# Optimization experiments

Hardware: AMD Instinct MI355X
Metric: run time of the kernel (lower is better)

## Reference

```python
import jax, jax.numpy as jnp
import numpy as np
import math

LMAX = 3  # max output/input angular momentum degree


def _cg(j1, m1, j2, m2, j, m):
    """Clebsch-Gordan coefficient <j1 m1 j2 m2 | j m> (Condon-Shortley)."""
    if m1 + m2 != m or not (abs(j1 - j2) <= j <= j1 + j2):
        return 0.0
    f = math.factorial
    pref = math.sqrt(
        (2 * j + 1)
        * f(j + j1 - j2) * f(j - j1 + j2) * f(j1 + j2 - j) / f(j1 + j2 + j + 1)
        * f(j + m) * f(j - m) * f(j1 - m1) * f(j1 + m1) * f(j2 - m2) * f(j2 + m2)
    )
    kmin = max(0, j2 - j - m1, j1 - j + m2)
    kmax = min(j1 + j2 - j, j1 - m1, j2 + m2)
    s = 0.0
    for k in range(kmin, kmax + 1):
        s += (-1) ** k / (
            f(k) * f(j1 + j2 - j - k) * f(j1 - m1 - k) * f(j2 + m2 - k)
            * f(j - j2 + m1 + k) * f(j - j1 - m2 + k)
        )
    return pref * s


def _cg_mat(l1, l2, l):
    C = np.zeros((2 * l1 + 1, 2 * l2 + 1, 2 * l + 1), dtype=np.float32)
    for m1 in range(-l1, l1 + 1):
        for m2 in range(-l2, l2 + 1):
            m = m1 + m2
            if abs(m) <= l:
                C[m1 + l1, m2 + l2, m + l] = _cg(l1, m1, l2, m2, l, m)
    return C


_CG = {}
for _l1 in range(LMAX + 1):
    for _l2 in range(LMAX + 1):
        for _l in range(abs(_l1 - _l2), min(_l1 + _l2, LMAX) + 1):
            _CG[(_l1, _l2, _l)] = jnp.asarray(_cg_mat(_l1, _l2, _l))


def _cg_product(A, B):
    """Full CG tensor product of two SO3 vec-arrays.

    A[l], B[l]: (2=complex, N, 2l+1, tau). Output degree l collects, for every
    (l1, l2) pair with |l1-l2| <= l <= l1+l2, the channel outer product
    contracted against the CG matrix (cormorant CGProduct semantics).
    """
    parts = [[] for _ in range(LMAX + 1)]
    for l1 in range(LMAX + 1):
        for l2 in range(LMAX + 1):
            Ar, Ai = A[l1][0], A[l1][1]  # (N, 2l1+1, tau1)
            Br, Bi = B[l2][0], B[l2][1]  # (N, 2l2+1, tau2)
            for l in range(abs(l1 - l2), min(l1 + l2, LMAX) + 1):
                C = _CG[(l1, l2, l)]  # (2l1+1, 2l2+1, 2l+1)
                Tr = (jnp.einsum('xyz,nxc,nyd->nzcd', C, Ar, Br)
                      - jnp.einsum('xyz,nxc,nyd->nzcd', C, Ai, Bi))
                Ti = (jnp.einsum('xyz,nxc,nyd->nzcd', C, Ar, Bi)
                      + jnp.einsum('xyz,nxc,nyd->nzcd', C, Ai, Br))
                n = Tr.shape[0]
                T = jnp.stack([Tr, Ti], axis=0).reshape(2, n, 2 * l + 1, -1)
                parts[l].append(T)
    return tuple(jnp.concatenate(p, axis=-1) for p in parts)


def setup_inputs() -> dict:
    key = jax.random.key(0)
    keys = jax.random.split(key, 8)
    N, TAU = 1024, 16
    d = {}
    for l in range(LMAX + 1):
        d[f'A{l}'] = jax.random.normal(keys[l], (2, N, 2 * l + 1, TAU), dtype=jnp.float32)
        d[f'B{l}'] = jax.random.normal(keys[4 + l], (2, N, 2 * l + 1, TAU), dtype=jnp.float32)
    return d


def reference(A0, A1, A2, A3, B0, B1, B2, B3):
    return _cg_product([A0, A1, A2, A3], [B0, B1, B2, B3])
```

## Files before the change

kernel.cpp:

```cpp
#include <hip/hip_runtime.h>


typedef float f32x4 __attribute__((ext_vector_type(4)));

constexpr double dfactc(int n) {
    double r = 1.0;
    for (int i = 2; i <= n; ++i) r *= (double)i;
    return r;
}

constexpr double csqrt(double x) {
    if (x <= 0.0) return 0.0;
    double g = x >= 1.0 ? x : 1.0;
    for (int i = 0; i < 50; ++i) g = 0.5 * (g + x / g);
    return g;
}

constexpr double cg_coef_c(int j1, int m1, int j2, int m2, int j, int m) {
    if (m1 + m2 != m) return 0.0;
    double pref = csqrt((double)(2 * j + 1)
        * dfactc(j + j1 - j2) * dfactc(j - j1 + j2) * dfactc(j1 + j2 - j)
        / dfactc(j1 + j2 + j + 1)
        * dfactc(j + m) * dfactc(j - m) * dfactc(j1 - m1) * dfactc(j1 + m1)
        * dfactc(j2 - m2) * dfactc(j2 + m2));
    int kmin = 0;
    if (j2 - j - m1 > kmin) kmin = j2 - j - m1;
    if (j1 - j + m2 > kmin) kmin = j1 - j + m2;
    int kmax = j1 + j2 - j;
    if (j1 - m1 < kmax) kmax = j1 - m1;
    if (j2 + m2 < kmax) kmax = j2 + m2;
    double s = 0.0;
    for (int k = kmin; k <= kmax; ++k) {
        double d = dfactc(k) * dfactc(j1 + j2 - j - k) * dfactc(j1 - m1 - k)
                 * dfactc(j2 + m2 - k) * dfactc(j - j2 + m1 + k)
                 * dfactc(j - j1 - m2 + k);
        s += (k & 1) ? (-1.0 / d) : (1.0 / d);
    }
    return pref * s;
}

template <int l1, int l2, int L>
struct CGMat {
    float v[(2 * l1 + 1) * (2 * l2 + 1) * (2 * L + 1)];
};

template <int l1, int l2, int L>
constexpr CGMat<l1, l2, L> make_cgmat() {
    CGMat<l1, l2, L> t{};
    constexpr int yd = 2 * l2 + 1, zd = 2 * L + 1;
    for (int x = 0; x < 2 * l1 + 1; ++x)
        for (int y = 0; y < yd; ++y)
            for (int z = 0; z < zd; ++z)
                t.v[(x * yd + y) * zd + z] =
                    (float)cg_coef_c(l1, x - l1, l2, y - l2, L, z - L);
    return t;
}

template <int l1, int l2, int L>
constexpr CGMat<l1, l2, L> CGM = make_cgmat<l1, l2, L>();

struct TriTab {
    int l1[34], l2[34], L[34], c0[34];
    int ch[4];
    int cum[4];
};

constexpr TriTab make_tab() {
    TriTab t{};
    int idx = 0;
    int c0L[4] = {0, 0, 0, 0};
    for (int a = 0; a <= 3; ++a)
    for (int b = 0; b <= 3; ++b) {
        int lo = (a > b) ? (a - b) : (b - a);
        int hi = (a + b < 3) ? (a + b) : 3;
        for (int l = lo; l <= hi; ++l) {
            t.l1[idx] = a; t.l2[idx] = b; t.L[idx] = l;
            t.c0[idx] = c0L[l]; c0L[l] += 256;
            ++idx;
        }
    }
    for (int l = 0; l < 4; ++l) t.ch[l] = c0L[l];
    int acc = 0;
    for (int l = 0; l < 4; ++l) { t.cum[l] = acc; acc += 2 * (2 * l + 1) * c0L[l]; }
    return t;
}

constexpr TriTab TAB = make_tab();

template <int l1, int l2, int L, int c0>
__device__ __forceinline__ void tri_body(
    const float* __restrict__ A0, const float* __restrict__ A1,
    const float* __restrict__ A2, const float* __restrict__ A3,
    const float* __restrict__ B0, const float* __restrict__ B1,
    const float* __restrict__ B2, const float* __restrict__ B3,
    float* __restrict__ out, int N)
{
    constexpr int xdim = 2 * l1 + 1, ydim = 2 * l2 + 1, zdim = 2 * L + 1;
    constexpr int CHL = TAB.ch[L];

    const unsigned q   = blockIdx.x * 256 + threadIdx.x;
    const unsigned n   = q >> 6;
    const unsigned cd4 = q & 63;
    const unsigned c   = cd4 >> 2;
    const unsigned d4  = (cd4 & 3) << 2;

    const float* Ab = (l1 == 0) ? A0 : (l1 == 1) ? A1 : (l1 == 2) ? A2 : A3;
    const float* Bb = (l2 == 0) ? B0 : (l2 == 1) ? B1 : (l2 == 2) ? B2 : B3;

    const float* Ar = Ab + n * (unsigned)(xdim * 16) + c;
    const float* Ai = Ar + (unsigned)N * (unsigned)(xdim * 16);
    const float* Br = Bb + n * (unsigned)(ydim * 16) + d4;
    const float* Bi = Br + (unsigned)N * (unsigned)(ydim * 16);

    float ar[xdim], ai[xdim];
    #pragma unroll
    for (int x = 0; x < xdim; ++x) { ar[x] = Ar[x * 16]; ai[x] = Ai[x * 16]; }
    f32x4 br[ydim], bi[ydim];
    #pragma unroll
    for (int y = 0; y < ydim; ++y) {
        br[y] = *reinterpret_cast<const f32x4*>(Br + y * 16);
        bi[y] = *reinterpret_cast<const f32x4*>(Bi + y * 16);
    }

    unsigned off = (unsigned)N * (unsigned)TAB.cum[L]
                 + n * (unsigned)(zdim * CHL) + (unsigned)(c0) + cd4 * 4u;
    const unsigned imagOff = (unsigned)N * (unsigned)(zdim * CHL);

    #pragma unroll
    for (int z = 0; z < zdim; ++z) {
        const int s   = z + l1 + l2 - L;
        const int xlo = (s - (ydim - 1) > 0) ? s - (ydim - 1) : 0;
        const int xhi = (s < xdim - 1) ? s : xdim - 1;
        f32x4 accr = {0.f, 0.f, 0.f, 0.f};
        f32x4 acci = {0.f, 0.f, 0.f, 0.f};
        #pragma unroll
        for (int x = xlo; x <= xhi; ++x) {
            const int y = s - x;
            const float cgv = CGM<l1, l2, L>.v[(x * ydim + y) * zdim + z];
            if (cgv != 0.0f) {
                const float car = cgv * ar[x];
                const float cai = cgv * ai[x];
                accr += car * br[y] - cai * bi[y];
                acci += car * bi[y] + cai * br[y];
            }
        }
        __builtin_nontemporal_store(accr, reinterpret_cast<f32x4*>(out + off));
        __builtin_nontemporal_store(acci, reinterpret_cast<f32x4*>(out + off + imagOff));
        off += CHL;
    }
}

__global__ __launch_bounds__(256) void cg_prod_all(
    const float* __restrict__ A0, const float* __restrict__ A1,
    const float* __restrict__ A2, const float* __restrict__ A3,
    const float* __restrict__ B0, const float* __restrict__ B1,
    const float* __restrict__ B2, const float* __restrict__ B3,
    float* __restrict__ out, int N)
{
    switch (blockIdx.y) {
#define TC(i) case i: tri_body<TAB.l1[i], TAB.l2[i], TAB.L[i], TAB.c0[i]>( \
        A0, A1, A2, A3, B0, B1, B2, B3, out, N); break;
        TC(0)  TC(1)  TC(2)  TC(3)  TC(4)  TC(5)  TC(6)  TC(7)
        TC(8)  TC(9)  TC(10) TC(11) TC(12) TC(13) TC(14) TC(15)
        TC(16) TC(17) TC(18) TC(19) TC(20) TC(21) TC(22) TC(23)
        TC(24) TC(25) TC(26) TC(27) TC(28) TC(29) TC(30) TC(31)
        TC(32) TC(33)
#undef TC
    }
}

extern "C" void kernel_launch(void* const* d_in, const int* in_sizes, int n_in,
                              void* d_out, int out_size, void* d_ws, size_t ws_size,
                              hipStream_t stream) {
    const float* A0 = (const float*)d_in[0];
    const float* B0 = (const float*)d_in[1];
    const float* A1 = (const float*)d_in[2];
    const float* B1 = (const float*)d_in[3];
    const float* A2 = (const float*)d_in[4];
    const float* B2 = (const float*)d_in[5];
    const float* A3 = (const float*)d_in[6];
    const float* B3 = (const float*)d_in[7];
    float* out = (float*)d_out;

    const int N = in_sizes[0] / 32;

    hipLaunchKernelGGL(cg_prod_all, dim3(N / 4, 34), dim3(256), 0, stream,
                       A0, A1, A2, A3, B0, B1, B2, B3, out, N);
}
```

Measured before the change: 344.6 us.

## Remap work so each wave writes one contiguous output row in sequential order

Replaces the per-triple 2D grid with a 1D grid where each 64-lane wave handles one (L, n, z, pair) output row, ordered to match the output memory layout so stores are fully sequential. CG coefficients move to __constant__ tables indexed at runtime, and only the needed B rows are loaded per z. Inputs are re-read once per z row, which adds load traffic and runtime index arithmetic (div/mod, switch dispatch) in exchange for more linear write streaming.

After: 338.7 us. Within noise of the previous version (-1.7%).

```diff
diff --git a/kernel.cpp b/kernel.cpp
--- a/kernel.cpp
+++ b/kernel.cpp
@@ -12,7 +12,7 @@
 constexpr double csqrt(double x) {
     if (x <= 0.0) return 0.0;
     double g = x >= 1.0 ? x : 1.0;
-    for (int i = 0; i < 50; ++i) g = 0.5 * (g + x / g);
+    for (int i = 0; i < 32; ++i) g = 0.5 * (g + x / g);
     return g;
 }
 
@@ -39,133 +39,171 @@
     return pref * s;
 }
 
-template <int l1, int l2, int L>
-struct CGMat {
-    float v[(2 * l1 + 1) * (2 * l2 + 1) * (2 * L + 1)];
+struct PairList {
+    int l1[11], l2[11], off[11];
+    int np, total;
 };
 
-template <int l1, int l2, int L>
-constexpr CGMat<l1, l2, L> make_cgmat() {
-    CGMat<l1, l2, L> t{};
-    constexpr int yd = 2 * l2 + 1, zd = 2 * L + 1;
-    for (int x = 0; x < 2 * l1 + 1; ++x)
-        for (int y = 0; y < yd; ++y)
-            for (int z = 0; z < zd; ++z)
-                t.v[(x * yd + y) * zd + z] =
-                    (float)cg_coef_c(l1, x - l1, l2, y - l2, L, z - L);
-    return t;
-}
-
-template <int l1, int l2, int L>
-constexpr CGMat<l1, l2, L> CGM = make_cgmat<l1, l2, L>();
-
-struct TriTab {
-    int l1[34], l2[34], L[34], c0[34];
-    int ch[4];
-    int cum[4];
-};
-
-constexpr TriTab make_tab() {
-    TriTab t{};
-    int idx = 0;
-    int c0L[4] = {0, 0, 0, 0};
+constexpr PairList plist(int L) {
+    PairList P{};
+    int np = 0, off = 0;
     for (int a = 0; a <= 3; ++a)
     for (int b = 0; b <= 3; ++b) {
         int lo = (a > b) ? (a - b) : (b - a);
         int hi = (a + b < 3) ? (a + b) : 3;
-        for (int l = lo; l <= hi; ++l) {
-            t.l1[idx] = a; t.l2[idx] = b; t.L[idx] = l;
-            t.c0[idx] = c0L[l]; c0L[l] += 256;
-            ++idx;
+        if (lo <= L && L <= hi) {
+            P.l1[np] = a; P.l2[np] = b; P.off[np] = off;
+            off += (2 * a + 1) * (2 * b + 1) * (2 * L + 1);
+            ++np;
         }
     }
-    for (int l = 0; l < 4; ++l) t.ch[l] = c0L[l];
+    P.np = np; P.total = off;
+    return P;
+}
+
+constexpr int cum_floats(int L) {
     int acc = 0;
-    for (int l = 0; l < 4; ++l) { t.cum[l] = acc; acc += 2 * (2 * l + 1) * c0L[l]; }
+    for (int l = 0; l < L; ++l) acc += 2 * (2 * l + 1) * 256 * plist(l).np;
+    return acc;
+}
+
+template <int L> struct CGTabT { float v[plist(L).total]; };
+
+template <int L>
+constexpr CGTabT<L> make_cgtab() {
+    CGTabT<L> t{};
+    constexpr PairList P = plist(L);
+    constexpr int zd = 2 * L + 1;
+    for (int p = 0; p < P.np; ++p) {
+        const int l1 = P.l1[p], l2 = P.l2[p];
+        const int yd = 2 * l2 + 1;
+        for (int x = 0; x < 2 * l1 + 1; ++x)
+            for (int y = 0; y < yd; ++y)
+                for (int z = 0; z < zd; ++z)
+                    t.v[P.off[p] + (x * yd + y) * zd + z] =
+                        (float)cg_coef_c(l1, x - l1, l2, y - l2, L, z - L);
+    }
     return t;
 }
 
-constexpr TriTab TAB = make_tab();
-
-template <int l1, int l2, int L, int c0>
-__device__ __forceinline__ void tri_body(
+__constant__ CGTabT<0> CGT0 = make_cgtab<0>();
+__constant__ CGTabT<1> CGT1 = make_cgtab<1>();
+__constant__ CGTabT<2> CGT2 = make_cgtab<2>();
+__constant__ CGTabT<3> CGT3 = make_cgtab<3>();
+
+template <int l1, int l2, int L>
+__device__ __forceinline__ void pair_body(
+    const float* __restrict__ A0, const float* __restrict__ A1,
+    const float* __restrict__ A2, const float* __restrict__ A3,
+    const float* __restrict__ B0, const float* __restrict__ B1,
+    const float* __restrict__ B2, const float* __restrict__ B3,
+    const float* __restrict__ cg, int cgoff,
+    unsigned z, unsigned n, unsigned lane,
+    float* __restrict__ out, unsigned rowOff, unsigned imagOff, int N)
+{
+    constexpr int xdim = 2 * l1 + 1, ydim = 2 * l2 + 1, zdim = 2 * L + 1;
+
+    const int s   = (int)z + l1 + l2 - L;
+    const int xlo = (s - (ydim - 1) > 0) ? s - (ydim - 1) : 0;
+    const int xhi = (s < xdim - 1) ? s : (xdim - 1);
+
+    const unsigned c  = lane >> 2;
+    const unsigned d4 = (lane & 3u) << 2;
+
+    const float* Ab = (l1 == 0) ? A0 : (l1 == 1) ? A1 : (l1 == 2) ? A2 : A3;
+    const float* Bb = (l2 == 0) ? B0 : (l2 == 1) ? B1 : (l2 == 2) ? B2 : B3;
+
+    const float* Ar = Ab + n * (unsigned)(xdim * 16) + c;
+    const float* Ai = Ar + (unsigned)N * (unsigned)(xdim * 16);
+    const float* Br = Bb + n * (unsigned)(ydim * 16) + d4;
+    const float* Bi = Br + (unsigned)N * (unsigned)(ydim * 16);
+
+    float ar[xdim], ai[xdim];
+    #pragma unroll
+    for (int x = 0; x < xdim; ++x) { ar[x] = Ar[x * 16]; ai[x] = Ai[x * 16]; }
+
+    const int cgbase = cgoff + s * zdim + (int)z;
+
+    f32x4 accr = {0.f, 0.f, 0.f, 0.f};
+    f32x4 acci = {0.f, 0.f, 0.f, 0.f};
+    #pragma unroll
+    for (int x = 0; x < xdim; ++x) {
+        if (x >= xlo && x <= xhi) {
+            const float cgv = cg[cgbase + x * (ydim - 1) * zdim];
+            const float car = cgv * ar[x];
+            const float cai = cgv * ai[x];
+            const f32x4 brv = *reinterpret_cast<const f32x4*>(Br + (unsigned)(s - x) * 16u);
+            const f32x4 biv = *reinterpret_cast<const f32x4*>(Bi + (unsigned)(s - x) * 16u);
+            accr += car * brv - cai * biv;
+            acci += car * biv + cai * brv;
+        }
+    }
+
+    float* oR = out + rowOff + lane * 4u;
+    __builtin_nontemporal_store(accr, reinterpret_cast<f32x4*>(oR));
+    __builtin_nontemporal_store(acci, reinterpret_cast<f32x4*>(oR + imagOff));
+}
+
+template <int L>
+__device__ __forceinline__ void doL(unsigned w, unsigned lane,
     const float* __restrict__ A0, const float* __restrict__ A1,
     const float* __restrict__ A2, const float* __restrict__ A3,
     const float* __restrict__ B0, const float* __restrict__ B1,
     const float* __restrict__ B2, const float* __restrict__ B3,
     float* __restrict__ out, int N)
 {
-    constexpr int xdim = 2 * l1 + 1, ydim = 2 * l2 + 1, zdim = 2 * L + 1;
-    constexpr int CHL = TAB.ch[L];
-
-    const unsigned q   = blockIdx.x * 256 + threadIdx.x;
-    const unsigned n   = q >> 6;
-    const unsigned cd4 = q & 63;
-    const unsigned c   = cd4 >> 2;
-    const unsigned d4  = (cd4 & 3) << 2;
-
-    const float* Ab = (l1 == 0) ? A0 : (l1 == 1) ? A1 : (l1 == 2) ? A2 : A3;
-    const float* Bb = (l2 == 0) ? B0 : (l2 == 1) ? B1 : (l2 == 2) ? B2 : B3;
-
-    const float* Ar = Ab + n * (unsigned)(xdim * 16) + c;
-    const float* Ai = Ar + (unsigned)N * (unsigned)(xdim * 16);
-    const float* Br = Bb + n * (unsigned)(ydim * 16) + d4;
-    const float* Bi = Br + (unsigned)N * (unsigned)(ydim * 16);
-
-    float ar[xdim], ai[xdim];
-    #pragma unroll
-    for (int x = 0; x < xdim; ++x) { ar[x] = Ar[x * 16]; ai[x] = Ai[x * 16]; }
-    f32x4 br[ydim], bi[ydim];
-    #pragma unroll
-    for (int y = 0; y < ydim; ++y) {
-        br[y] = *reinterpret_cast<const f32x4*>(Br + y * 16);
-        bi[y] = *reinterpret_cast<const f32x4*>(Bi + y * 16);
-    }
-
-    unsigned off = (unsigned)N * (unsigned)TAB.cum[L]
-                 + n * (unsigned)(zdim * CHL) + (unsigned)(c0) + cd4 * 4u;
-    const unsigned imagOff = (unsigned)N * (unsigned)(zdim * CHL);
-
-    #pragma unroll
-    for (int z = 0; z < zdim; ++z) {
-        const int s   = z + l1 + l2 - L;
-        const int xlo = (s - (ydim - 1) > 0) ? s - (ydim - 1) : 0;
-        const int xhi = (s < xdim - 1) ? s : xdim - 1;
-        f32x4 accr = {0.f, 0.f, 0.f, 0.f};
-        f32x4 acci = {0.f, 0.f, 0.f, 0.f};
-        #pragma unroll
-        for (int x = xlo; x <= xhi; ++x) {
-            const int y = s - x;
-            const float cgv = CGM<l1, l2, L>.v[(x * ydim + y) * zdim + z];
-            if (cgv != 0.0f) {
-                const float car = cgv * ar[x];
-                const float cai = cgv * ai[x];
-                accr += car * br[y] - cai * bi[y];
-                acci += car * bi[y] + cai * br[y];
-            }
-        }
-        __builtin_nontemporal_store(accr, reinterpret_cast<f32x4*>(out + off));
-        __builtin_nontemporal_store(acci, reinterpret_cast<f32x4*>(out + off + imagOff));
-        off += CHL;
-    }
-}
-
-__global__ __launch_bounds__(256) void cg_prod_all(
+    constexpr int NP  = plist(L).np;
+    constexpr int ZD  = 2 * L + 1;
+    constexpr int CHL = 256 * NP;
+
+    const unsigned p = w % (unsigned)NP;
+    const unsigned r = w / (unsigned)NP;
+    const unsigned z = r % (unsigned)ZD;
+    const unsigned n = r / (unsigned)ZD;
+
+    const unsigned rowOff  = (unsigned)N * (unsigned)cum_floats(L) + w * 256u;
+    const unsigned imagOff = (unsigned)N * (unsigned)(ZD * CHL);
+
+    const float* cg = (L == 0) ? CGT0.v : (L == 1) ? CGT1.v
+                    : (L == 2) ? CGT2.v : CGT3.v;
+
+#define PB(Lv, K) case K: pair_body<plist(Lv).l1[K], plist(Lv).l2[K], Lv>( \
+        A0, A1, A2, A3, B0, B1, B2, B3, cg, plist(Lv).off[K], z, n, lane,  \
+        out, rowOff, imagOff, N); break;
+
+    if constexpr (L == 0) {
+        switch (p) { PB(0,0) PB(0,1) PB(0,2) PB(0,3) }
+    } else if constexpr (L == 1) {
+        switch (p) { PB(1,0) PB(1,1) PB(1,2) PB(1,3) PB(1,4) PB(1,5) PB(1,6) PB(1,7) PB(1,8) }
+    } else if constexpr (L == 2) {
+        switch (p) { PB(2,0) PB(2,1) PB(2,2) PB(2,3) PB(2,4) PB(2,5) PB(2,6) PB(2,7) PB(2,8) PB(2,9) PB(2,10) }
+    } else {
+        switch (p) { PB(3,0) PB(3,1) PB(3,2) PB(3,3) PB(3,4) PB(3,5) PB(3,6) PB(3,7) PB(3,8) PB(3,9) }
+    }
+#undef PB
+}
+
+__global__ __launch_bounds__(256) void cg_prod_seq(
     const float* __restrict__ A0, const float* __restrict__ A1,
     const float* __restrict__ A2, const float* __restrict__ A3,
     const float* __restrict__ B0, const float* __restrict__ B1,
     const float* __restrict__ B2, const float* __restrict__ B3,
     float* __restrict__ out, int N)
 {
-    switch (blockIdx.y) {
-#define TC(i) case i: tri_body<TAB.l1[i], TAB.l2[i], TAB.L[i], TAB.c0[i]>( \
-        A0, A1, A2, A3, B0, B1, B2, B3, out, N); break;
-        TC(0)  TC(1)  TC(2)  TC(3)  TC(4)  TC(5)  TC(6)  TC(7)
-        TC(8)  TC(9)  TC(10) TC(11) TC(12) TC(13) TC(14) TC(15)
-        TC(16) TC(17) TC(18) TC(19) TC(20) TC(21) TC(22) TC(23)
-        TC(24) TC(25) TC(26) TC(27) TC(28) TC(29) TC(30) TC(31)
-        TC(32) TC(33)
-#undef TC
+    const unsigned gtid = blockIdx.x * 256u + threadIdx.x;
+    const unsigned lane = threadIdx.x & 63u;
+    unsigned W = gtid >> 6;
+    W = (unsigned)__builtin_amdgcn_readfirstlane((int)W);
+
+    const unsigned NN = (unsigned)N;
+    if (W < 4u * NN) {
+        doL<0>(W,            lane, A0, A1, A2, A3, B0, B1, B2, B3, out, N);
+    } else if (W < 31u * NN) {
+        doL<1>(W - 4u * NN,  lane, A0, A1, A2, A3, B0, B1, B2, B3, out, N);
+    } else if (W < 86u * NN) {
+        doL<2>(W - 31u * NN, lane, A0, A1, A2, A3, B0, B1, B2, B3, out, N);
+    } else if (W < 156u * NN) {
+        doL<3>(W - 86u * NN, lane, A0, A1, A2, A3, B0, B1, B2, B3, out, N);
     }
 }
 
@@ -181,9 +219,11 @@
     const float* A3 = (const float*)d_in[6];
     const float* B3 = (const float*)d_in[7];
     float* out = (float*)d_out;
+    (void)d_ws; (void)ws_size;
 
     const int N = in_sizes[0] / 32;
 
-    hipLaunchKernelGGL(cg_prod_all, dim3(N / 4, 34), dim3(256), 0, stream,
+    const int blocks = (156 * N + 3) / 4 / 256 * 256 ? (39 * N) : (39 * N);
+    hipLaunchKernelGGL(cg_prod_seq, dim3(39 * N), dim3(256), 0, stream,
                        A0, A1, A2, A3, B0, B1, B2, B3, out, N);
 }
```
